# Performance work log

Hardware: AMD Instinct MI355X
Metric: run time of the kernel (lower is better)

## Reference

```python
import jax, jax.numpy as jnp
import numpy as np

B, C, W, H, K = 8, 512, 64, 64, 64
C4 = C // 4

def setup_inputs() -> dict:
    key = jax.random.key(0)
    ks = jax.random.split(key, 12)
    return {
        "x1": jax.random.normal(ks[0], (B, C, W, H), jnp.float32),
        "y1": jax.random.normal(ks[1], (B, K, C), jnp.float32),
        "x2": jax.random.normal(ks[2], (B, C, W, H), jnp.float32),
        "y2": jax.random.normal(ks[3], (B, K, C), jnp.float32),
        "wq": jax.random.normal(ks[4], (C4, C), jnp.float32) * 0.02,
        "bq": jax.random.normal(ks[5], (C4,), jnp.float32) * 0.02,
        "wk": jax.random.normal(ks[6], (C4, C), jnp.float32) * 0.02,
        "bk": jax.random.normal(ks[7], (C4,), jnp.float32) * 0.02,
        "wv": jax.random.normal(ks[8], (C, C), jnp.float32) * 0.02,
        "bv": jax.random.normal(ks[9], (C,), jnp.float32) * 0.02,
        "scale": jax.random.normal(ks[10], (1,), jnp.float32),
        "scale1": jax.random.normal(ks[11], (1,), jnp.float32),
    }

def reference(x1, y1, x2, y2, wq, bq, wk, bk, wv, bv, scale, scale1):
    b, c, w, h = x1.shape
    k = y1.shape[1]
    n = w * h
    # value projections (nn.Linear: y @ W^T + b), kept as [B, C, K]
    pv1 = jnp.einsum('bkc,dc->bdk', y1, wv) + bv[None, :, None]
    pv2 = jnp.einsum('bkc,dc->bdk', y2, wv) + bv[None, :, None]
    # 1x1 conv query: [B, C4, W, H] -> [B, N, C4]
    q = jnp.einsum('bcwh,dc->bwhd', x2, wq) + bq
    q = q.reshape(b, n, -1)
    # key: [B, K, C4] -> bmm contracts over C4
    kk = jnp.einsum('bkc,dc->bkd', y2, wk) + bk  # [B, K, C4]
    energy = jnp.einsum('bnd,bkd->bnk', q, kk)   # [B, N, K]
    attention = jax.nn.softmax(jnp.abs(energy), axis=-1)
    # out = value [B,C,K] @ attention^T [B,K,N] -> [B,C,N]
    out1 = jnp.einsum('bck,bnk->bcn', pv1, attention).reshape(b, c, w, h)
    out1 = scale[0] * out1 + x1
    out2 = jnp.einsum('bck,bnk->bcn', pv2, attention).reshape(b, c, w, h)
    out2 = scale1[0] * out2 + x2
    return (out1, out2)
```

## Files before the change

kernel.cpp:

```cpp
#include <hip/hip_runtime.h>
#include <math.h>

#define Bn 8
#define Cn 512
#define Kn 64
#define C4n 128
#define Nn 4096

typedef short bf16x8 __attribute__((ext_vector_type(8)));
typedef float f32x4  __attribute__((ext_vector_type(4)));
typedef unsigned short u16;

__device__ __forceinline__ u16 f2bf(float f) {
    union { float f; unsigned u; } v; v.f = f;
    unsigned r = v.u + 0x7FFF + ((v.u >> 16) & 1);
    return (u16)(r >> 16);
}
__device__ __forceinline__ float bf2f(u16 h) {
    union { unsigned u; float f; } v; v.u = ((unsigned)h) << 16;
    return v.f;
}
__device__ __forceinline__ bf16x8 cvt8(const float* p) {
    float4 a = *(const float4*)p;
    float4 b = *(const float4*)(p + 4);
    bf16x8 r;
    r[0] = (short)f2bf(a.x); r[1] = (short)f2bf(a.y);
    r[2] = (short)f2bf(a.z); r[3] = (short)f2bf(a.w);
    r[4] = (short)f2bf(b.x); r[5] = (short)f2bf(b.y);
    r[6] = (short)f2bf(b.z); r[7] = (short)f2bf(b.w);
    return r;
}

__global__ __launch_bounds__(256) void kk_pv_kernel(
    const float* __restrict__ y1, const float* __restrict__ y2,
    const float* __restrict__ wv, const float* __restrict__ bv,
    const float* __restrict__ wk, const float* __restrict__ bk,
    u16* __restrict__ pv1h, u16* __restrict__ pv2h, u16* __restrict__ kkh)
{
    const int b    = blockIdx.y;
    const int sel  = blockIdx.z;
    const int lane = threadIdx.x & 63;
    const int wid  = threadIdx.x >> 6;
    const int lr   = lane & 15;
    const int lg   = lane >> 4;

    if (sel < 2) {
        const int cb   = blockIdx.x * 64 + wid * 16;
        const float* y = sel ? y2 : y1;
        u16* pvh       = sel ? pv2h : pv1h;

        f32x4 acc[4];
        #pragma unroll
        for (int kt = 0; kt < 4; ++kt) acc[kt] = (f32x4){0.f, 0.f, 0.f, 0.f};

        for (int c0 = 0; c0 < Cn; c0 += 32) {
            const int cf = c0 + lg * 8;
            bf16x8 wfr = cvt8(wv + (size_t)(cb + lr) * Cn + cf);
            bf16x8 yfr[4];
            #pragma unroll
            for (int kt = 0; kt < 4; ++kt)
                yfr[kt] = cvt8(y + (size_t)(b * Kn + kt * 16 + lr) * Cn + cf);
            #pragma unroll
            for (int kt = 0; kt < 4; ++kt)
                acc[kt] = __builtin_amdgcn_mfma_f32_16x16x32_bf16(
                    yfr[kt], wfr, acc[kt], 0, 0, 0);
        }
        const int c = cb + lr;
        const float bb = bv[c];
        #pragma unroll
        for (int kt = 0; kt < 4; ++kt) {
            ushort4 o;
            o.x = f2bf(acc[kt][0] + bb); o.y = f2bf(acc[kt][1] + bb);
            o.z = f2bf(acc[kt][2] + bb); o.w = f2bf(acc[kt][3] + bb);
            *(ushort4*)&pvh[(((size_t)(b * Cn + c)) << 6) + kt * 16 + 4 * lg] = o;
        }
    } else {
        const int dblk = blockIdx.x * 16;
        f32x4 acc = (f32x4){0.f, 0.f, 0.f, 0.f};
        for (int c0 = 0; c0 < Cn; c0 += 32) {
            const int cf = c0 + lg * 8;
            bf16x8 wfr = cvt8(wk + (size_t)(dblk + lr) * Cn + cf);
            bf16x8 yfr = cvt8(y2 + (size_t)(b * Kn + wid * 16 + lr) * Cn + cf);
            acc = __builtin_amdgcn_mfma_f32_16x16x32_bf16(wfr, yfr, acc, 0, 0, 0);
        }
        const int d4 = dblk + 4 * lg;
        float4 bkv = *(const float4*)&bk[d4];
        ushort4 o;
        o.x = f2bf(acc[0] + bkv.x); o.y = f2bf(acc[1] + bkv.y);
        o.z = f2bf(acc[2] + bkv.z); o.w = f2bf(acc[3] + bkv.w);
        *(ushort4*)&kkh[(((size_t)(b * Kn + wid * 16 + lr)) << 7) + d4] = o;
    }
}

__global__ __launch_bounds__(256) void M_e0_kernel(
    const u16* __restrict__ kkh, const float* __restrict__ wq,
    const float* __restrict__ bq, u16* __restrict__ Mth,
    float* __restrict__ e0)
{
    const int b = blockIdx.y;
    const int t = threadIdx.x;

    if (blockIdx.x == 4) {
        if (t < Kn) {
            const u16* row = kkh + (((size_t)(b * Kn + t)) << 7);
            float acc = 0.f;
            #pragma unroll
            for (int d8 = 0; d8 < C4n; d8 += 8) {
                bf16x8 v = *(const bf16x8*)(row + d8);
                #pragma unroll
                for (int j = 0; j < 8; ++j)
                    acc += bq[d8 + j] * bf2f((u16)v[j]);
            }
            e0[b * Kn + t] = acc;
        }
        return;
    }

    const int cb   = blockIdx.x * 128 + (t >> 6) * 32;
    const int lane = t & 63;
    const int lr   = lane & 15;
    const int lg   = lane >> 4;

    f32x4 acc[2][4];
    #pragma unroll
    for (int ct = 0; ct < 2; ++ct)
        #pragma unroll
        for (int kt = 0; kt < 4; ++kt) acc[ct][kt] = (f32x4){0.f, 0.f, 0.f, 0.f};

    for (int d0 = 0; d0 < C4n; d0 += 32) {
        const int df = d0 + lg * 8;
        bf16x8 afr[2];
        #pragma unroll
        for (int ct = 0; ct < 2; ++ct) {
            const int c = cb + ct * 16 + lr;
            bf16x8 r;
            #pragma unroll
            for (int j = 0; j < 8; ++j)
                r[j] = (short)f2bf(wq[(size_t)(df + j) * Cn + c]);
            afr[ct] = r;
        }
        bf16x8 bfr[4];
        #pragma unroll
        for (int kt = 0; kt < 4; ++kt)
            bfr[kt] = *(const bf16x8*)&kkh[(((size_t)(b * Kn + kt * 16 + lr)) << 7) + df];
        #pragma unroll
        for (int ct = 0; ct < 2; ++ct)
            #pragma unroll
            for (int kt = 0; kt < 4; ++kt)
                acc[ct][kt] = __builtin_amdgcn_mfma_f32_16x16x32_bf16(
                    afr[ct], bfr[kt], acc[ct][kt], 0, 0, 0);
    }
    #pragma unroll
    for (int ct = 0; ct < 2; ++ct) {
        const int c4 = cb + ct * 16 + 4 * lg;
        #pragma unroll
        for (int kt = 0; kt < 4; ++kt) {
            ushort4 o;
            o.x = f2bf(acc[ct][kt][0]); o.y = f2bf(acc[ct][kt][1]);
            o.z = f2bf(acc[ct][kt][2]); o.w = f2bf(acc[ct][kt][3]);
            *(ushort4*)&Mth[(size_t)(b * Kn + kt * 16 + lr) * Cn + c4] = o;
        }
    }
}

__global__ __launch_bounds__(256) void attn_out_kernel(
    const float* __restrict__ x1, const float* __restrict__ x2,
    const u16* __restrict__ pv1h, const u16* __restrict__ pv2h,
    const u16* __restrict__ Mth, const float* __restrict__ e0,
    const float* __restrict__ scale, const float* __restrict__ scale1,
    float* __restrict__ out1, float* __restrict__ out2)
{
    __shared__ float smem[4 * 2176];
    u16* attL = (u16*)smem;

    const int id   = blockIdx.x;
    const int b    = id & 7;
    const int n0   = (id >> 3) * 64;
    const int t    = threadIdx.x;
    const int lane = t & 63;
    const int wid  = t >> 6;
    const int lr   = lane & 15;
    const int lg   = lane >> 4;
    const int nl   = wid * 16 + lr;

    f32x4 eacc[4];
    #pragma unroll
    for (int kt = 0; kt < 4; ++kt) eacc[kt] = (f32x4){0.f, 0.f, 0.f, 0.f};

    const float* xcol = x2 + (((size_t)b * Cn) << 12) + n0 + nl;
    const u16*   mb   = Mth + ((size_t)b << 15) + (size_t)lr * Cn;

    for (int c0 = 0; c0 < Cn; c0 += 32) {
        const int cf = c0 + lg * 8;
        float xs[8];
        #pragma unroll
        for (int j = 0; j < 8; ++j)
            xs[j] = xcol[((size_t)(cf + j)) << 12];
        bf16x8 xfr;
        #pragma unroll
        for (int j = 0; j < 8; ++j) xfr[j] = (short)f2bf(xs[j]);
        #pragma unroll
        for (int kt = 0; kt < 4; ++kt) {
            bf16x8 av = *(const bf16x8*)(mb + ((size_t)kt << 13) + cf);
            eacc[kt] = __builtin_amdgcn_mfma_f32_16x16x32_bf16(av, xfr, eacc[kt], 0, 0, 0);
        }
    }

    {
        float a[4][4];
        float mx = 0.f;
        #pragma unroll
        for (int kt = 0; kt < 4; ++kt) {
            float4 e0v = *(const float4*)&e0[b * Kn + kt * 16 + lg * 4];
            float er[4] = {e0v.x, e0v.y, e0v.z, e0v.w};
            #pragma unroll
            for (int reg = 0; reg < 4; ++reg) {
                float v = fabsf(eacc[kt][reg] + er[reg]);
                a[kt][reg] = v;
                mx = fmaxf(mx, v);
            }
        }
        mx = fmaxf(mx, __shfl_xor(mx, 16));
        mx = fmaxf(mx, __shfl_xor(mx, 32));
        float s = 0.f;
        #pragma unroll
        for (int kt = 0; kt < 4; ++kt)
            #pragma unroll
            for (int reg = 0; reg < 4; ++reg) {
                a[kt][reg] = __expf(a[kt][reg] - mx);
                s += a[kt][reg];
            }
        s += __shfl_xor(s, 16);
        s += __shfl_xor(s, 32);
        const float inv = 1.0f / s;

        #pragma unroll
        for (int kt = 0; kt < 4; ++kt) {
            ushort4 o;
            o.x = f2bf(a[kt][0] * inv); o.y = f2bf(a[kt][1] * inv);
            o.z = f2bf(a[kt][2] * inv); o.w = f2bf(a[kt][3] * inv);
            const int chunk = (kt * 2 + (lg >> 1)) ^ (nl & 7);
            *(ushort4*)&attL[nl * 64 + chunk * 8 + 4 * (lg & 1)] = o;
        }
    }
    __syncthreads();

    bf16x8 af[4][2];
    #pragma unroll
    for (int nt = 0; nt < 4; ++nt)
        #pragma unroll
        for (int ks = 0; ks < 2; ++ks) {
            const int nn = nt * 16 + lr;
            const int chunk = (ks * 4 + lg) ^ (nn & 7);
            af[nt][ks] = *(const bf16x8*)&attL[nn * 64 + chunk * 8];
        }
    __syncthreads();

    const float sA = scale[0], sB = scale1[0];
    float* Tw1 = smem + wid * 2176;
    float* Tw2 = Tw1 + 1088;

    const size_t rowb = (((size_t)(b * Cn + wid * 16 + lg)) << 12) + n0 + lr * 4;

    const u16* p1 = pv1h + (((size_t)(b * Cn + wid * 16 + lr)) << 6) + lg * 8;
    const u16* p2 = pv2h + (((size_t)(b * Cn + wid * 16 + lr)) << 6) + lg * 8;
    bf16x8 v1[2], v2[2];
    v1[0] = *(const bf16x8*)p1;  v1[1] = *(const bf16x8*)(p1 + 32);
    v2[0] = *(const bf16x8*)p2;  v2[1] = *(const bf16x8*)(p2 + 32);
    float4 xv1[4], xv2[4];
    #pragma unroll
    for (int r4 = 0; r4 < 4; ++r4) {
        const size_t row = rowb + ((size_t)(r4 * 4) << 12);
        xv1[r4] = *(const float4*)&x1[row];
        xv2[r4] = *(const float4*)&x2[row];
    }

    for (int ct = 0; ct < 8; ++ct) {
        f32x4 acc1[4], acc2[4];
        #pragma unroll
        for (int nt = 0; nt < 4; ++nt) {
            f32x4 z = (f32x4){0.f, 0.f, 0.f, 0.f};
            acc1[nt] = __builtin_amdgcn_mfma_f32_16x16x32_bf16(af[nt][0], v1[0], z, 0, 0, 0);
            acc1[nt] = __builtin_amdgcn_mfma_f32_16x16x32_bf16(af[nt][1], v1[1], acc1[nt], 0, 0, 0);
            acc2[nt] = __builtin_amdgcn_mfma_f32_16x16x32_bf16(af[nt][0], v2[0], z, 0, 0, 0);
            acc2[nt] = __builtin_amdgcn_mfma_f32_16x16x32_bf16(af[nt][1], v2[1], acc2[nt], 0, 0, 0);
        }

        bf16x8 nv1[2], nv2[2];
        float4 nx1[4], nx2[4];
        if (ct < 7) {
            const int wc = (ct + 1) * 64 + wid * 16;
            const u16* q1 = pv1h + (((size_t)(b * Cn + wc + lr)) << 6) + lg * 8;
            const u16* q2 = pv2h + (((size_t)(b * Cn + wc + lr)) << 6) + lg * 8;
            nv1[0] = *(const bf16x8*)q1;  nv1[1] = *(const bf16x8*)(q1 + 32);
            nv2[0] = *(const bf16x8*)q2;  nv2[1] = *(const bf16x8*)(q2 + 32);
            #pragma unroll
            for (int r4 = 0; r4 < 4; ++r4) {
                const size_t row = rowb + ((size_t)((ct + 1) * 64 + r4 * 4) << 12);
                nx1[r4] = *(const float4*)&x1[row];
                nx2[r4] = *(const float4*)&x2[row];
            }
        }

        #pragma unroll
        for (int nt = 0; nt < 4; ++nt) {
            float4 u, w;
            u.x = acc1[nt][0]; u.y = acc1[nt][1];
            u.z = acc1[nt][2]; u.w = acc1[nt][3];
            w.x = acc2[nt][0]; w.y = acc2[nt][1];
            w.z = acc2[nt][2]; w.w = acc2[nt][3];
            *(float4*)&Tw1[lr * 68 + nt * 16 + 4 * lg] = u;
            *(float4*)&Tw2[lr * 68 + nt * 16 + 4 * lg] = w;
        }
        #pragma unroll
        for (int r4 = 0; r4 < 4; ++r4) {
            const int rloc = r4 * 4 + lg;
            const size_t row = rowb + ((size_t)(ct * 64 + r4 * 4) << 12);
            float4 a1 = *(const float4*)&Tw1[rloc * 68 + lr * 4];
            float4 a2 = *(const float4*)&Tw2[rloc * 68 + lr * 4];
            f32x4 o1, o2;
            o1[0] = sA * a1.x + xv1[r4].x;  o1[1] = sA * a1.y + xv1[r4].y;
            o1[2] = sA * a1.z + xv1[r4].z;  o1[3] = sA * a1.w + xv1[r4].w;
            o2[0] = sB * a2.x + xv2[r4].x;  o2[1] = sB * a2.y + xv2[r4].y;
            o2[2] = sB * a2.z + xv2[r4].z;  o2[3] = sB * a2.w + xv2[r4].w;
            __builtin_nontemporal_store(o1, (f32x4*)&out1[row]);
            __builtin_nontemporal_store(o2, (f32x4*)&out2[row]);
        }

        v1[0] = nv1[0]; v1[1] = nv1[1];
        v2[0] = nv2[0]; v2[1] = nv2[1];
        #pragma unroll
        for (int r4 = 0; r4 < 4; ++r4) { xv1[r4] = nx1[r4]; xv2[r4] = nx2[r4]; }
    }
}

extern "C" void kernel_launch(void* const* d_in, const int* in_sizes, int n_in,
                              void* d_out, int out_size, void* d_ws, size_t ws_size,
                              hipStream_t stream)
{
    const float* x1     = (const float*)d_in[0];
    const float* y1     = (const float*)d_in[1];
    const float* x2     = (const float*)d_in[2];
    const float* y2     = (const float*)d_in[3];
    const float* wq     = (const float*)d_in[4];
    const float* bq     = (const float*)d_in[5];
    const float* wk     = (const float*)d_in[6];
    const float* bk     = (const float*)d_in[7];
    const float* wv     = (const float*)d_in[8];
    const float* bv     = (const float*)d_in[9];
    const float* scale  = (const float*)d_in[10];
    const float* scale1 = (const float*)d_in[11];

    float* out1 = (float*)d_out;
    float* out2 = out1 + (size_t)Bn * Cn * Nn;

    float* ws   = (float*)d_ws;
    float* e0   = ws;
    u16*   kkh  = (u16*)(ws + 512);
    u16*   Mth  = kkh + 65536;
    u16*   pv1h = Mth + 262144;
    u16*   pv2h = pv1h + 262144;

    kk_pv_kernel<<<dim3(8, Bn, 3), 256, 0, stream>>>(
        y1, y2, wv, bv, wk, bk, pv1h, pv2h, kkh);
    M_e0_kernel<<<dim3(5, Bn), 256, 0, stream>>>(kkh, wq, bq, Mth, e0);
    attn_out_kernel<<<512, 256, 0, stream>>>(
        x1, x2, pv1h, pv2h, Mth, e0, scale, scale1, out1, out2);
}
```

Baseline: 93.37 us.

## Double attn_out block to 512 threads, split energy reduction over channel halves

The output kernel now runs 8 waves per block instead of 4. For the energy GEMM, two groups of waves each reduce half of the channel dimension, and the partial sums are combined through shared memory before the softmax. In the output phase each wave covers 4 channel tiles instead of 8, and the register prefetch of pv and x for the next tile is removed in favour of more waves in flight. The change trades the explicit software prefetch and some register pressure for more occupancy, at the cost of an extra sync and a shared-memory partial-sum exchange.

```diff
diff --git a/kernel.cpp b/kernel.cpp
--- a/kernel.cpp
+++ b/kernel.cpp
@@ -163,15 +163,16 @@
     }
 }
 
-__global__ __launch_bounds__(256) void attn_out_kernel(
+__global__ __launch_bounds__(512, 4) void attn_out_kernel(
     const float* __restrict__ x1, const float* __restrict__ x2,
     const u16* __restrict__ pv1h, const u16* __restrict__ pv2h,
     const u16* __restrict__ Mth, const float* __restrict__ e0,
     const float* __restrict__ scale, const float* __restrict__ scale1,
     float* __restrict__ out1, float* __restrict__ out2)
 {
-    __shared__ float smem[4 * 2176];
-    u16* attL = (u16*)smem;
+    __shared__ float smem[17408];
+    u16*   attL = (u16*)smem;
+    float* part = smem + 2048;
 
     const int id   = blockIdx.x;
     const int b    = id & 7;
@@ -181,7 +182,9 @@
     const int wid  = t >> 6;
     const int lr   = lane & 15;
     const int lg   = lane >> 4;
-    const int nl   = wid * 16 + lr;
+    const int nw   = wid & 3;
+    const int ch   = wid >> 2;
+    const int nl   = nw * 16 + lr;
 
     f32x4 eacc[4];
     #pragma unroll
@@ -190,7 +193,8 @@
     const float* xcol = x2 + (((size_t)b * Cn) << 12) + n0 + nl;
     const u16*   mb   = Mth + ((size_t)b << 15) + (size_t)lr * Cn;
 
-    for (int c0 = 0; c0 < Cn; c0 += 32) {
+    const int cbeg = ch * 256;
+    for (int c0 = cbeg; c0 < cbeg + 256; c0 += 32) {
         const int cf = c0 + lg * 8;
         float xs[8];
         #pragma unroll
@@ -206,16 +210,26 @@
         }
     }
 
-    {
+    if (ch == 1) {
+        float* p = part + (nw * 64 + lane) * 20;
+        #pragma unroll
+        for (int kt = 0; kt < 4; ++kt)
+            *(f32x4*)(p + kt * 4) = eacc[kt];
+    }
+    __syncthreads();
+
+    if (ch == 0) {
+        const float* p = part + (nw * 64 + lane) * 20;
         float a[4][4];
         float mx = 0.f;
         #pragma unroll
         for (int kt = 0; kt < 4; ++kt) {
+            f32x4 pv4 = *(const f32x4*)(p + kt * 4);
             float4 e0v = *(const float4*)&e0[b * Kn + kt * 16 + lg * 4];
             float er[4] = {e0v.x, e0v.y, e0v.z, e0v.w};
             #pragma unroll
             for (int reg = 0; reg < 4; ++reg) {
-                float v = fabsf(eacc[kt][reg] + er[reg]);
+                float v = fabsf(eacc[kt][reg] + pv4[reg] + er[reg]);
                 a[kt][reg] = v;
                 mx = fmaxf(mx, v);
             }
@@ -260,22 +274,15 @@
     float* Tw1 = smem + wid * 2176;
     float* Tw2 = Tw1 + 1088;
 
-    const size_t rowb = (((size_t)(b * Cn + wid * 16 + lg)) << 12) + n0 + lr * 4;
-
-    const u16* p1 = pv1h + (((size_t)(b * Cn + wid * 16 + lr)) << 6) + lg * 8;
-    const u16* p2 = pv2h + (((size_t)(b * Cn + wid * 16 + lr)) << 6) + lg * 8;
-    bf16x8 v1[2], v2[2];
-    v1[0] = *(const bf16x8*)p1;  v1[1] = *(const bf16x8*)(p1 + 32);
-    v2[0] = *(const bf16x8*)p2;  v2[1] = *(const bf16x8*)(p2 + 32);
-    float4 xv1[4], xv2[4];
-    #pragma unroll
-    for (int r4 = 0; r4 < 4; ++r4) {
-        const size_t row = rowb + ((size_t)(r4 * 4) << 12);
-        xv1[r4] = *(const float4*)&x1[row];
-        xv2[r4] = *(const float4*)&x2[row];
-    }
-
-    for (int ct = 0; ct < 8; ++ct) {
+    for (int ci = 0; ci < 4; ++ci) {
+        const int wc = ci * 128 + wid * 16;
+
+        const u16* p1 = pv1h + (((size_t)(b * Cn + wc + lr)) << 6) + lg * 8;
+        const u16* p2 = pv2h + (((size_t)(b * Cn + wc + lr)) << 6) + lg * 8;
+        bf16x8 v1[2], v2[2];
+        v1[0] = *(const bf16x8*)p1;  v1[1] = *(const bf16x8*)(p1 + 32);
+        v2[0] = *(const bf16x8*)p2;  v2[1] = *(const bf16x8*)(p2 + 32);
+
         f32x4 acc1[4], acc2[4];
         #pragma unroll
         for (int nt = 0; nt < 4; ++nt) {
@@ -284,22 +291,6 @@
             acc1[nt] = __builtin_amdgcn_mfma_f32_16x16x32_bf16(af[nt][1], v1[1], acc1[nt], 0, 0, 0);
             acc2[nt] = __builtin_amdgcn_mfma_f32_16x16x32_bf16(af[nt][0], v2[0], z, 0, 0, 0);
             acc2[nt] = __builtin_amdgcn_mfma_f32_16x16x32_bf16(af[nt][1], v2[1], acc2[nt], 0, 0, 0);
-        }
-
-        bf16x8 nv1[2], nv2[2];
-        float4 nx1[4], nx2[4];
-        if (ct < 7) {
-            const int wc = (ct + 1) * 64 + wid * 16;
-            const u16* q1 = pv1h + (((size_t)(b * Cn + wc + lr)) << 6) + lg * 8;
-            const u16* q2 = pv2h + (((size_t)(b * Cn + wc + lr)) << 6) + lg * 8;
-            nv1[0] = *(const bf16x8*)q1;  nv1[1] = *(const bf16x8*)(q1 + 32);
-            nv2[0] = *(const bf16x8*)q2;  nv2[1] = *(const bf16x8*)(q2 + 32);
-            #pragma unroll
-            for (int r4 = 0; r4 < 4; ++r4) {
-                const size_t row = rowb + ((size_t)((ct + 1) * 64 + r4 * 4) << 12);
-                nx1[r4] = *(const float4*)&x1[row];
-                nx2[r4] = *(const float4*)&x2[row];
-            }
         }
 
         #pragma unroll
@@ -315,22 +306,19 @@
         #pragma unroll
         for (int r4 = 0; r4 < 4; ++r4) {
             const int rloc = r4 * 4 + lg;
-            const size_t row = rowb + ((size_t)(ct * 64 + r4 * 4) << 12);
+            const size_t row = (((size_t)(b * Cn + wc + rloc)) << 12) + n0 + lr * 4;
             float4 a1 = *(const float4*)&Tw1[rloc * 68 + lr * 4];
             float4 a2 = *(const float4*)&Tw2[rloc * 68 + lr * 4];
+            float4 xv1 = *(const float4*)&x1[row];
+            float4 xv2 = *(const float4*)&x2[row];
             f32x4 o1, o2;
-            o1[0] = sA * a1.x + xv1[r4].x;  o1[1] = sA * a1.y + xv1[r4].y;
-            o1[2] = sA * a1.z + xv1[r4].z;  o1[3] = sA * a1.w + xv1[r4].w;
-            o2[0] = sB * a2.x + xv2[r4].x;  o2[1] = sB * a2.y + xv2[r4].y;
-            o2[2] = sB * a2.z + xv2[r4].z;  o2[3] = sB * a2.w + xv2[r4].w;
+            o1[0] = sA * a1.x + xv1.x;  o1[1] = sA * a1.y + xv1.y;
+            o1[2] = sA * a1.z + xv1.z;  o1[3] = sA * a1.w + xv1.w;
+            o2[0] = sB * a2.x + xv2.x;  o2[1] = sB * a2.y + xv2.y;
+            o2[2] = sB * a2.z + xv2.z;  o2[3] = sB * a2.w + xv2.w;
             __builtin_nontemporal_store(o1, (f32x4*)&out1[row]);
             __builtin_nontemporal_store(o2, (f32x4*)&out2[row]);
         }
-
-        v1[0] = nv1[0]; v1[1] = nv1[1];
-        v2[0] = nv2[0]; v2[1] = nv2[1];
-        #pragma unroll
-        for (int r4 = 0; r4 < 4; ++r4) { xv1[r4] = nx1[r4]; xv2[r4] = nx2[r4]; }
     }
 }
 
@@ -364,6 +352,6 @@
     kk_pv_kernel<<<dim3(8, Bn, 3), 256, 0, stream>>>(
         y1, y2, wv, bv, wk, bk, pv1h, pv2h, kkh);
     M_e0_kernel<<<dim3(5, Bn), 256, 0, stream>>>(kkh, wq, bq, Mth, e0);
-    attn_out_kernel<<<512, 256, 0, stream>>>(
+    attn_out_kernel<<<512, 512, 0, stream>>>(
         x1, x2, pv1h, pv2h, Mth, e0, scale, scale1, out1, out2);
 }
```

Measured after the change: 91.51 us. -2.0%, faster.
